# Optimization experiments

Hardware: AMD Instinct MI355X
Metric: run time of the kernel (lower is better)

## Reference

```python
import jax, jax.numpy as jnp
import numpy as np

N_NODES = 100000
N_EDGES = 1600000
D_IN, D_HID, D_OUT = 128, 128, 64


def setup_inputs() -> dict:
    key = jax.random.key(0)
    k1, k2, k3, k4 = jax.random.split(key, 4)
    x = jax.random.normal(k1, (N_NODES, D_IN), dtype=jnp.float32)
    edge_index = jax.random.randint(k2, (2, N_EDGES), 0, N_NODES, dtype=jnp.int64)
    # Glorot-style weights, zero bias (GCNConv defaults: weight + bias)
    W1 = jax.random.normal(k3, (D_IN, D_HID), dtype=jnp.float32) * (1.0 / np.sqrt(D_IN))
    b1 = jnp.zeros((D_HID,), dtype=jnp.float32)
    W2 = jax.random.normal(k4, (D_HID, D_OUT), dtype=jnp.float32) * (1.0 / np.sqrt(D_HID))
    b2 = jnp.zeros((D_OUT,), dtype=jnp.float32)
    return {"x": x, "edge_index": edge_index, "W1": W1, "b1": b1, "W2": W2, "b2": b2}


def reference(x, edge_index, W1, b1, W2, b2):
    n = x.shape[0]
    src, dst = edge_index[0], edge_index[1]
    # GCN symmetric normalization, add_self_loops=False
    ones = jnp.ones((src.shape[0],), dtype=x.dtype)
    deg = jax.ops.segment_sum(ones, dst, num_segments=n)
    deg_inv_sqrt = jnp.where(deg > 0, jax.lax.rsqrt(jnp.maximum(deg, 1.0)), 0.0)
    norm = deg_inv_sqrt[src] * deg_inv_sqrt[dst]  # [E]

    def gcn_conv(h, W, b):
        h = h @ W                                   # [N, d_out] transform first
        msg = h[src] * norm[:, None]                # [E, d_out] gather + scale
        agg = jax.ops.segment_sum(msg, dst, num_segments=n)  # scatter-add
        return agg + b

    h = jax.nn.relu(gcn_conv(x, W1, b1))
    # dropout(p=0.6) is identity in eval mode (training=False)
    return gcn_conv(h, W2, b2)
```

## Files before the change

kernel.cpp:

```cpp
#include <hip/hip_runtime.h>

#define N_NODES 100000
#define N_EDGES 1600000
#define NBUCK 391
#define CHUNKA 8192
#define NBLKA 196

typedef __bf16 bf16x8 __attribute__((ext_vector_type(8)));
typedef float f32x4 __attribute__((ext_vector_type(4)));

__device__ inline unsigned short bf1(float a) {
    unsigned u = __builtin_bit_cast(unsigned, a);
    u = (u + 0x7FFF + ((u >> 16) & 1)) >> 16;
    return (unsigned short)u;
}
__device__ inline unsigned bfpack(float a, float b) {
    unsigned ua = __builtin_bit_cast(unsigned, a);
    unsigned ub = __builtin_bit_cast(unsigned, b);
    ua = (ua + 0x7FFF + ((ua >> 16) & 1)) >> 16;
    ub = (ub + 0x7FFF + ((ub >> 16) & 1)) >> 16;
    return ua | (ub << 16);
}
__device__ inline float bf2f(unsigned short u) {
    return __builtin_bit_cast(float, ((unsigned)u) << 16);
}

__global__ __launch_bounds__(256) void bhist_kernel(const int* __restrict__ ei,
                                                    int* __restrict__ bhist) {
    __shared__ int hist[NBUCK];
    const int t = threadIdx.x;
    const int e0 = blockIdx.x * CHUNKA;
    const int n  = min(CHUNKA, N_EDGES - e0);
    for (int i = t; i < NBUCK; i += 256) hist[i] = 0;
    __syncthreads();
    for (int i = t; i < n; i += 256) {
        int dst = ei[N_EDGES + e0 + i];
        atomicAdd(&hist[dst >> 8], 1);
    }
    __syncthreads();
    for (int i = t; i < NBUCK; i += 256)
        if (hist[i]) atomicAdd(&bhist[i], hist[i]);
}

__global__ __launch_bounds__(512) void prep_kernel(const int* __restrict__ bhist,
                                                   int* __restrict__ boffs,
                                                   const float* __restrict__ W1,
                                                   const float* __restrict__ W2,
                                                   unsigned short* __restrict__ Wt1,
                                                   unsigned short* __restrict__ Wt2) {
    const int t = threadIdx.x;
    if (blockIdx.x == 0) {
        __shared__ int s[512];
        int v = (t < NBUCK) ? bhist[t] : 0;
        s[t] = v;
        __syncthreads();
#pragma unroll
        for (int off = 1; off < 512; off <<= 1) {
            int tv = (t >= off) ? s[t - off] : 0;
            __syncthreads();
            s[t] += tv;
            __syncthreads();
        }
        if (t < NBUCK) boffs[t] = s[t] - v;
        if (t == NBUCK - 1) boffs[NBUCK] = s[t];
    } else if (blockIdx.x == 1) {
        for (int i = t; i < 128 * 128; i += 512) {
            int k = i >> 7, n = i & 127;
            Wt1[n * 128 + k] = bf1(W1[i]);
        }
    } else {
        for (int i = t; i < 128 * 64; i += 512) {
            int k = i >> 6, n = i & 63;
            Wt2[n * 128 + k] = bf1(W2[i]);
        }
    }
}

__global__ __launch_bounds__(256) void binA_kernel(const int* __restrict__ ei,
                                                   const int* __restrict__ boffs,
                                                   int* __restrict__ bcur,
                                                   unsigned* __restrict__ epk) {
    __shared__ int hist[NBUCK], base[NBUCK], cur[NBUCK];
    const int t = threadIdx.x;
    const int e0 = blockIdx.x * CHUNKA;
    const int n  = min(CHUNKA, N_EDGES - e0);
    for (int i = t; i < NBUCK; i += 256) hist[i] = 0;
    __syncthreads();
    for (int i = t; i < n; i += 256) {
        int dst = ei[N_EDGES + e0 + i];
        atomicAdd(&hist[dst >> 8], 1);
    }
    __syncthreads();
    for (int i = t; i < NBUCK; i += 256) {
        int h = hist[i];
        base[i] = boffs[i] + (h ? atomicAdd(&bcur[i], h) : 0);
        cur[i]  = 0;
    }
    __syncthreads();
    for (int i = t; i < n; i += 256) {
        int src = ei[e0 + i];
        int dst = ei[N_EDGES + e0 + i];
        int b   = dst >> 8;
        int r   = atomicAdd(&cur[b], 1);
        epk[base[b] + r] = ((unsigned)src << 8) | (unsigned)(dst & 255);
    }
}

__global__ __launch_bounds__(256) void binB_kernel(const unsigned* __restrict__ epk,
                                                   const int* __restrict__ boffs,
                                                   int* __restrict__ deg,
                                                   float* __restrict__ dis,
                                                   int* __restrict__ offs,
                                                   int* __restrict__ srcn) {
    __shared__ int cnt[256], s[256], loff[256];
    const int b  = blockIdx.x;
    const int t  = threadIdx.x;
    const int n0 = b << 8;
    const int base = boffs[b];
    const int end  = boffs[b + 1];
    cnt[t] = 0;
    __syncthreads();
    for (int e = base + t; e < end; e += 256)
        atomicAdd(&cnt[epk[e] & 255u], 1);
    __syncthreads();
    int v = cnt[t];
    s[t] = v;
    __syncthreads();
#pragma unroll
    for (int off = 1; off < 256; off <<= 1) {
        int tv = (t >= off) ? s[t - off] : 0;
        __syncthreads();
        s[t] += tv;
        __syncthreads();
    }
    loff[t] = s[t] - v;
    {
        int node = n0 + t;
        if (node < N_NODES) {
            deg[node]  = v;
            dis[node]  = (v > 0) ? rsqrtf((float)v) : 0.0f;
            offs[node] = base + loff[t];
        }
    }
    cnt[t] = 0;
    __syncthreads();
    for (int e = base + t; e < end; e += 256) {
        unsigned p = epk[e];
        int li  = (int)(p & 255u);
        int r   = atomicAdd(&cnt[li], 1);
        srcn[base + loff[li] + r] = (int)(p >> 8);
    }
}

__global__ __launch_bounds__(256) void gemm1_kernel(const float* __restrict__ x,
                                                    const unsigned short* __restrict__ Wt1,
                                                    const float* __restrict__ dis,
                                                    unsigned short* __restrict__ h1b) {
    __shared__ unsigned short Asm[64][136];
    __shared__ float diss[64];
    const int t = threadIdx.x;
    const int node0 = blockIdx.x * 64;

#pragma unroll
    for (int c = 0; c < 4; ++c) {
        int i = c * 256 + t;
        int row = i >> 4, ko = (i & 15) * 8;
        int gn = node0 + row;
        float4 v0 = make_float4(0, 0, 0, 0), v1 = v0;
        if (gn < N_NODES) {
            const float* p = x + (size_t)gn * 128 + ko;
            v0 = *(const float4*)p;
            v1 = *(const float4*)(p + 4);
        }
        uint4 o;
        o.x = bfpack(v0.x, v0.y); o.y = bfpack(v0.z, v0.w);
        o.z = bfpack(v1.x, v1.y); o.w = bfpack(v1.z, v1.w);
        *(uint4*)&Asm[row][ko] = o;
    }
    if (t < 64) {
        int gn = node0 + t;
        diss[t] = (gn < N_NODES) ? dis[gn] : 0.0f;
    }
    __syncthreads();

    const int wv = t >> 6, ln = t & 63;
    const int lc = ln & 15, q = ln >> 4;
    const int n0 = wv * 32;

    bf16x8 bfr[2][4];
#pragma unroll
    for (int nt = 0; nt < 2; ++nt)
#pragma unroll
        for (int k = 0; k < 4; ++k)
            bfr[nt][k] = *(const bf16x8*)(Wt1 + (size_t)(n0 + nt * 16 + lc) * 128 + k * 32 + q * 8);

    f32x4 acc[4][2];
#pragma unroll
    for (int m = 0; m < 4; ++m)
#pragma unroll
        for (int nt = 0; nt < 2; ++nt) acc[m][nt] = (f32x4)(0.0f);

#pragma unroll
    for (int k = 0; k < 4; ++k) {
        bf16x8 af[4];
#pragma unroll
        for (int m = 0; m < 4; ++m)
            af[m] = *(const bf16x8*)&Asm[m * 16 + lc][k * 32 + q * 8];
#pragma unroll
        for (int m = 0; m < 4; ++m)
#pragma unroll
            for (int nt = 0; nt < 2; ++nt)
                acc[m][nt] = __builtin_amdgcn_mfma_f32_16x16x32_bf16(af[m], bfr[nt][k], acc[m][nt], 0, 0, 0);
    }

#pragma unroll
    for (int m = 0; m < 4; ++m)
#pragma unroll
        for (int r = 0; r < 4; ++r) {
            int lr = m * 16 + q * 4 + r;
            int gn = node0 + lr;
            if (gn < N_NODES) {
                float dv = diss[lr];
#pragma unroll
                for (int nt = 0; nt < 2; ++nt)
                    h1b[(size_t)gn * 128 + n0 + nt * 16 + lc] = bf1(acc[m][nt][r] * dv);
            }
        }
}

__global__ __launch_bounds__(256) void agg1gemm2_kernel(const int* __restrict__ srcn,
                                                        const int* __restrict__ offs,
                                                        const int* __restrict__ deg,
                                                        const float* __restrict__ dis,
                                                        const unsigned* __restrict__ h1b,
                                                        const float* __restrict__ b1,
                                                        const unsigned short* __restrict__ Wt2,
                                                        unsigned short* __restrict__ h2b) {
    __shared__ unsigned short Zs[64][136];
    __shared__ float diss[64];
    __shared__ int offs_s[64], deg_s[64];
    const int t = threadIdx.x;
    const int node0 = blockIdx.x * 64;
    if (t < 64) {
        int gn = node0 + t;
        bool ok = gn < N_NODES;
        offs_s[t] = ok ? offs[gn] : 0;
        deg_s[t]  = ok ? deg[gn] : 0;
        diss[t]   = ok ? dis[gn] : 0.0f;
    }
    __syncthreads();

    const int wv = t >> 6, ln = t & 63;
    float2 bb = *(const float2*)(b1 + ln * 2);

    for (int i = 0; i < 16; ++i) {
        int lr  = wv * 16 + i;
        int beg = offs_s[lr];
        int d   = deg_s[lr];
        float dv = diss[lr];
        float ax = 0.0f, ay = 0.0f;
#pragma unroll 4
        for (int k = 0; k < d; ++k) {
            int src = srcn[beg + k];
            unsigned v = h1b[(size_t)src * 64 + ln];
            ax += __builtin_bit_cast(float, v << 16);
            ay += __builtin_bit_cast(float, v & 0xFFFF0000u);
        }
        float z0 = fmaxf(dv * ax + bb.x, 0.0f);
        float z1 = fmaxf(dv * ay + bb.y, 0.0f);
        *(unsigned*)&Zs[lr][ln * 2] = bfpack(z0, z1);
    }
    __syncthreads();

    const int lc = ln & 15, q = ln >> 4;
    const int n0 = wv * 16;

    bf16x8 bfr[4];
#pragma unroll
    for (int k = 0; k < 4; ++k)
        bfr[k] = *(const bf16x8*)(Wt2 + (size_t)(n0 + lc) * 128 + k * 32 + q * 8);

    f32x4 acc[4];
#pragma unroll
    for (int m = 0; m < 4; ++m) acc[m] = (f32x4)(0.0f);

#pragma unroll
    for (int k = 0; k < 4; ++k) {
        bf16x8 af[4];
#pragma unroll
        for (int m = 0; m < 4; ++m)
            af[m] = *(const bf16x8*)&Zs[m * 16 + lc][k * 32 + q * 8];
#pragma unroll
        for (int m = 0; m < 4; ++m)
            acc[m] = __builtin_amdgcn_mfma_f32_16x16x32_bf16(af[m], bfr[k], acc[m], 0, 0, 0);
    }

#pragma unroll
    for (int m = 0; m < 4; ++m)
#pragma unroll
        for (int r = 0; r < 4; ++r) {
            int lr = m * 16 + q * 4 + r;
            int gn = node0 + lr;
            if (gn < N_NODES) {
                float dv = diss[lr];
                h2b[(size_t)gn * 64 + n0 + lc] = bf1(acc[m][r] * dv);
            }
        }
}

__global__ __launch_bounds__(256) void agg2_kernel(const int* __restrict__ srcn,
                                                   const int* __restrict__ offs,
                                                   const int* __restrict__ deg,
                                                   const float* __restrict__ dis,
                                                   const unsigned short* __restrict__ h2b,
                                                   const float* __restrict__ b2,
                                                   float* __restrict__ out) {
    int wave = (blockIdx.x * 256 + threadIdx.x) >> 6;
    int lane = threadIdx.x & 63;
    if (wave >= N_NODES) return;
    int beg = offs[wave];
    int d   = deg[wave];
    float dv = dis[wave];
    float acc = 0.0f;
#pragma unroll 4
    for (int k = 0; k < d; ++k) {
        int src = srcn[beg + k];
        acc += bf2f(h2b[(size_t)src * 64 + lane]);
    }
    out[(size_t)wave * 64 + lane] = dv * acc + b2[lane];
}

extern "C" void kernel_launch(void* const* d_in, const int* in_sizes, int n_in,
                              void* d_out, int out_size, void* d_ws, size_t ws_size,
                              hipStream_t stream) {
    const float* x  = (const float*)d_in[0];
    const int*   ei = (const int*)d_in[1];
    const float* W1 = (const float*)d_in[2];
    const float* b1 = (const float*)d_in[3];
    const float* W2 = (const float*)d_in[4];
    const float* b2 = (const float*)d_in[5];
    float* out = (float*)d_out;

    char* ws = (char*)d_ws;
    int*   bhist = (int*)(ws);
    int*   bcur  = (int*)(ws + (size_t)4 * 1024);
    int*   boffs = (int*)(ws + (size_t)8 * 1024);
    int*   deg   = (int*)(ws + (size_t)16 * 1024);
    int*   offs  = (int*)(ws + (size_t)512 * 1024);
    float* dis   = (float*)(ws + (size_t)1024 * 1024);
    unsigned short* Wt1 = (unsigned short*)(ws + (size_t)1536 * 1024);
    unsigned short* Wt2 = (unsigned short*)(ws + (size_t)1600 * 1024);
    unsigned* epk = (unsigned*)(ws + (size_t)2560 * 1024);
    int*   srcn  = (int*)(ws + (size_t)9216 * 1024);
    unsigned short* h1b = (unsigned short*)(ws + (size_t)16 * 1024 * 1024);
    unsigned short* h2b = (unsigned short*)(ws + (size_t)48 * 1024 * 1024);

    hipMemsetAsync(ws, 0, (size_t)8 * 1024, stream);

    bhist_kernel<<<NBLKA, 256, 0, stream>>>(ei, bhist);
    prep_kernel<<<3, 512, 0, stream>>>(bhist, boffs, W1, W2, Wt1, Wt2);
    binA_kernel<<<NBLKA, 256, 0, stream>>>(ei, boffs, bcur, epk);
    binB_kernel<<<NBUCK, 256, 0, stream>>>(epk, boffs, deg, dis, offs, srcn);
    gemm1_kernel<<<(N_NODES + 63) / 64, 256, 0, stream>>>(x, Wt1, dis, h1b);
    agg1gemm2_kernel<<<(N_NODES + 63) / 64, 256, 0, stream>>>(srcn, offs, deg, dis,
                                                              (const unsigned*)h1b, b1, Wt2, h2b);
    agg2_kernel<<<(N_NODES * 64 + 255) / 256, 256, 0, stream>>>(srcn, offs, deg, dis, h2b, b2, out);
}
```

Baseline: 318.8 us.

## Stage neighbor lists in LDS and split edges across wave halves in aggregation

Both aggregation kernels now copy the block's contiguous CSR source-index range into shared memory when it fits (falling back to global reads otherwise). Each wave splits a node's edge list between its two 32-lane halves, so every lane loads wider vectors (uint2 or unsigned) and two edges are processed in parallel. The partial sums are then combined with a cross-half shuffle. agg2 is restructured from one wave per node to a block of 64 nodes, 16 per wave. This aims to raise memory-level parallelism and cut redundant index loads, at the cost of extra LDS use, a shuffle reduction and divergence on odd-degree tails.

```diff
diff --git a/kernel.cpp b/kernel.cpp
--- a/kernel.cpp
+++ b/kernel.cpp
@@ -5,6 +5,7 @@
 #define NBUCK 391
 #define CHUNKA 8192
 #define NBLKA 196
+#define ECAP 2048
 
 typedef __bf16 bf16x8 __attribute__((ext_vector_type(8)));
 typedef float f32x4 __attribute__((ext_vector_type(4)));
@@ -24,6 +25,8 @@
 __device__ inline float bf2f(unsigned short u) {
     return __builtin_bit_cast(float, ((unsigned)u) << 16);
 }
+__device__ inline float bflo(unsigned v) { return __builtin_bit_cast(float, v << 16); }
+__device__ inline float bfhi(unsigned v) { return __builtin_bit_cast(float, v & 0xFFFF0000u); }
 
 __global__ __launch_bounds__(256) void bhist_kernel(const int* __restrict__ ei,
                                                     int* __restrict__ bhist) {
@@ -239,6 +242,7 @@
     __shared__ unsigned short Zs[64][136];
     __shared__ float diss[64];
     __shared__ int offs_s[64], deg_s[64];
+    __shared__ int esrc[ECAP];
     const int t = threadIdx.x;
     const int node0 = blockIdx.x * 64;
     if (t < 64) {
@@ -249,26 +253,69 @@
         diss[t]   = ok ? dis[gn] : 0.0f;
     }
     __syncthreads();
+    const int lastv = min(63, N_NODES - 1 - node0);
+    const int eBase = offs_s[0];
+    const int eCnt  = offs_s[lastv] + deg_s[lastv] - eBase;
+    const bool staged = (eCnt <= ECAP);
+    if (staged) {
+        for (int i = t; i < eCnt; i += 256) esrc[i] = srcn[eBase + i];
+    }
+    __syncthreads();
 
     const int wv = t >> 6, ln = t & 63;
-    float2 bb = *(const float2*)(b1 + ln * 2);
+    const int c = ln & 31;
+    const int half = ln >> 5;
+    const uint2* __restrict__ h1v = (const uint2*)h1b;
+    float4 bb = *(const float4*)(b1 + 4 * c);
 
     for (int i = 0; i < 16; ++i) {
-        int lr  = wv * 16 + i;
-        int beg = offs_s[lr];
-        int d   = deg_s[lr];
-        float dv = diss[lr];
-        float ax = 0.0f, ay = 0.0f;
+        int lr = wv * 16 + i;
+        int d  = deg_s[lr];
+        float f0 = 0.0f, f1 = 0.0f, f2 = 0.0f, f3 = 0.0f;
+        if (staged) {
+            int bh = offs_s[lr] - eBase + half;
+            int dh = d >> 1;
 #pragma unroll 4
-        for (int k = 0; k < d; ++k) {
-            int src = srcn[beg + k];
-            unsigned v = h1b[(size_t)src * 64 + ln];
-            ax += __builtin_bit_cast(float, v << 16);
-            ay += __builtin_bit_cast(float, v & 0xFFFF0000u);
-        }
-        float z0 = fmaxf(dv * ax + bb.x, 0.0f);
-        float z1 = fmaxf(dv * ay + bb.y, 0.0f);
-        *(unsigned*)&Zs[lr][ln * 2] = bfpack(z0, z1);
+            for (int k = 0; k < dh; ++k) {
+                int s = esrc[bh + 2 * k];
+                uint2 v = h1v[(size_t)s * 32 + c];
+                f0 += bflo(v.x); f1 += bfhi(v.x);
+                f2 += bflo(v.y); f3 += bfhi(v.y);
+            }
+            if ((d & 1) && half == 0) {
+                int s = esrc[offs_s[lr] - eBase + d - 1];
+                uint2 v = h1v[(size_t)s * 32 + c];
+                f0 += bflo(v.x); f1 += bfhi(v.x);
+                f2 += bflo(v.y); f3 += bfhi(v.y);
+            }
+        } else {
+            int bh = offs_s[lr] + half;
+            int dh = d >> 1;
+#pragma unroll 4
+            for (int k = 0; k < dh; ++k) {
+                int s = srcn[bh + 2 * k];
+                uint2 v = h1v[(size_t)s * 32 + c];
+                f0 += bflo(v.x); f1 += bfhi(v.x);
+                f2 += bflo(v.y); f3 += bfhi(v.y);
+            }
+            if ((d & 1) && half == 0) {
+                int s = srcn[offs_s[lr] + d - 1];
+                uint2 v = h1v[(size_t)s * 32 + c];
+                f0 += bflo(v.x); f1 += bfhi(v.x);
+                f2 += bflo(v.y); f3 += bfhi(v.y);
+            }
+        }
+        f0 += __shfl_xor(f0, 32);
+        f1 += __shfl_xor(f1, 32);
+        f2 += __shfl_xor(f2, 32);
+        f3 += __shfl_xor(f3, 32);
+        if (half == 0) {
+            float dv = diss[lr];
+            uint2 o;
+            o.x = bfpack(fmaxf(dv * f0 + bb.x, 0.0f), fmaxf(dv * f1 + bb.y, 0.0f));
+            o.y = bfpack(fmaxf(dv * f2 + bb.z, 0.0f), fmaxf(dv * f3 + bb.w, 0.0f));
+            *(uint2*)&Zs[lr][c * 4] = o;
+        }
     }
     __syncthreads();
 
@@ -312,22 +359,82 @@
                                                    const int* __restrict__ offs,
                                                    const int* __restrict__ deg,
                                                    const float* __restrict__ dis,
-                                                   const unsigned short* __restrict__ h2b,
+                                                   const unsigned* __restrict__ h2b,
                                                    const float* __restrict__ b2,
                                                    float* __restrict__ out) {
-    int wave = (blockIdx.x * 256 + threadIdx.x) >> 6;
-    int lane = threadIdx.x & 63;
-    if (wave >= N_NODES) return;
-    int beg = offs[wave];
-    int d   = deg[wave];
-    float dv = dis[wave];
-    float acc = 0.0f;
+    __shared__ float diss[64];
+    __shared__ int offs_s[64], deg_s[64];
+    __shared__ int esrc[ECAP];
+    const int t = threadIdx.x;
+    const int node0 = blockIdx.x * 64;
+    if (t < 64) {
+        int gn = node0 + t;
+        bool ok = gn < N_NODES;
+        offs_s[t] = ok ? offs[gn] : 0;
+        deg_s[t]  = ok ? deg[gn] : 0;
+        diss[t]   = ok ? dis[gn] : 0.0f;
+    }
+    __syncthreads();
+    const int lastv = min(63, N_NODES - 1 - node0);
+    const int eBase = offs_s[0];
+    const int eCnt  = offs_s[lastv] + deg_s[lastv] - eBase;
+    const bool staged = (eCnt <= ECAP);
+    if (staged) {
+        for (int i = t; i < eCnt; i += 256) esrc[i] = srcn[eBase + i];
+    }
+    __syncthreads();
+
+    const int wv = t >> 6, ln = t & 63;
+    const int c = ln & 31;
+    const int half = ln >> 5;
+    float2 bb = *(const float2*)(b2 + 2 * c);
+
+    for (int i = 0; i < 16; ++i) {
+        int lr = wv * 16 + i;
+        int d  = deg_s[lr];
+        float f0 = 0.0f, f1 = 0.0f;
+        if (staged) {
+            int bh = offs_s[lr] - eBase + half;
+            int dh = d >> 1;
 #pragma unroll 4
-    for (int k = 0; k < d; ++k) {
-        int src = srcn[beg + k];
-        acc += bf2f(h2b[(size_t)src * 64 + lane]);
-    }
-    out[(size_t)wave * 64 + lane] = dv * acc + b2[lane];
+            for (int k = 0; k < dh; ++k) {
+                int s = esrc[bh + 2 * k];
+                unsigned v = h2b[(size_t)s * 32 + c];
+                f0 += bflo(v); f1 += bfhi(v);
+            }
+            if ((d & 1) && half == 0) {
+                int s = esrc[offs_s[lr] - eBase + d - 1];
+                unsigned v = h2b[(size_t)s * 32 + c];
+                f0 += bflo(v); f1 += bfhi(v);
+            }
+        } else {
+            int bh = offs_s[lr] + half;
+            int dh = d >> 1;
+#pragma unroll 4
+            for (int k = 0; k < dh; ++k) {
+                int s = srcn[bh + 2 * k];
+                unsigned v = h2b[(size_t)s * 32 + c];
+                f0 += bflo(v); f1 += bfhi(v);
+            }
+            if ((d & 1) && half == 0) {
+                int s = srcn[offs_s[lr] + d - 1];
+                unsigned v = h2b[(size_t)s * 32 + c];
+                f0 += bflo(v); f1 += bfhi(v);
+            }
+        }
+        f0 += __shfl_xor(f0, 32);
+        f1 += __shfl_xor(f1, 32);
+        if (half == 0) {
+            int gn = node0 + lr;
+            if (gn < N_NODES) {
+                float dv = diss[lr];
+                float2 o;
+                o.x = dv * f0 + bb.x;
+                o.y = dv * f1 + bb.y;
+                *(float2*)(out + (size_t)gn * 64 + 2 * c) = o;
+            }
+        }
+    }
 }
 
 extern "C" void kernel_launch(void* const* d_in, const int* in_sizes, int n_in,
@@ -364,5 +471,6 @@
     gemm1_kernel<<<(N_NODES + 63) / 64, 256, 0, stream>>>(x, Wt1, dis, h1b);
     agg1gemm2_kernel<<<(N_NODES + 63) / 64, 256, 0, stream>>>(srcn, offs, deg, dis,
                                                               (const unsigned*)h1b, b1, Wt2, h2b);
-    agg2_kernel<<<(N_NODES * 64 + 255) / 256, 256, 0, stream>>>(srcn, offs, deg, dis, h2b, b2, out);
-}
+    agg2_kernel<<<(N_NODES + 63) / 64, 256, 0, stream>>>(srcn, offs, deg, dis,
+                                                         (const unsigned*)h2b, b2, out);
+}
```

Result: faster. 296.6 us (-7.0%).
